# Kernel optimization log

Measured on AMD Instinct MI355X. Metric: run time of the kernel, lower is better.

The kernel has to match this reference:

```python
import jax, jax.numpy as jnp
import numpy as np

NUM_GROUPS = 32
EPS = 1e-6

def group_norm(x, gamma, beta):
    b, c, h, w = x.shape
    xg = x.reshape(b, NUM_GROUPS, c // NUM_GROUPS, h, w)
    mean = xg.mean(axis=(2, 3, 4), keepdims=True)
    var = xg.var(axis=(2, 3, 4), keepdims=True)
    xg = (xg - mean) * jax.lax.rsqrt(var + EPS)
    x = xg.reshape(b, c, h, w)
    return x * gamma[None, :, None, None] + beta[None, :, None, None]

def conv1x1(x, w, b):
    # x: [B,C,H,W], w: [Cout,Cin], b: [Cout]
    return jnp.einsum('bchw,oc->bohw', x, w) + b[None, :, None, None]

def setup_inputs() -> dict:
    key = jax.random.key(0)
    ks = jax.random.split(key, 11)
    B, C, H, W = 4, 512, 64, 64
    s = 1.0 / np.sqrt(C)
    return {
        'x': jax.random.normal(ks[0], (B, C, H, W), dtype=jnp.float32),
        'gn_gamma': jnp.ones((C,), jnp.float32),
        'gn_beta': jnp.zeros((C,), jnp.float32),
        'wq': jax.random.normal(ks[1], (C, C), jnp.float32) * s,
        'bq': jnp.zeros((C,), jnp.float32),
        'wk': jax.random.normal(ks[2], (C, C), jnp.float32) * s,
        'bk': jnp.zeros((C,), jnp.float32),
        'wv': jax.random.normal(ks[3], (C, C), jnp.float32) * s,
        'bv': jnp.zeros((C,), jnp.float32),
        'wo': jax.random.normal(ks[4], (C, C), jnp.float32) * s,
        'bo': jnp.zeros((C,), jnp.float32),
    }

def reference(x, gn_gamma, gn_beta, wq, bq, wk, bk, wv, bv, wo, bo):
    b, c, H, W = x.shape
    h = group_norm(x, gn_gamma, gn_beta)
    q = conv1x1(h, wq, bq).reshape(b, c, H * W).transpose(0, 2, 1)  # [B, HW, C]
    k = conv1x1(h, wk, bk).reshape(b, c, H * W)                      # [B, C, HW]
    v = conv1x1(h, wv, bv).reshape(b, c, H * W).transpose(0, 2, 1)  # [B, HW, C]
    attn = jnp.einsum('bnc,bcm->bnm', q, k) * (c ** -0.5)            # [B, HW, HW]
    attn = jax.nn.softmax(attn, axis=-1)
    out = jnp.einsum('bnm,bmc->bnc', attn, v)                        # [B, HW, C]
    out = out.transpose(0, 2, 1).reshape(b, c, H, W)
    return x + conv1x1(out, wo, bo)
```

## Files before the change

### kernel.cpp

```cpp
#include <hip/hip_runtime.h>
#include <cstdint>
#include <cstddef>

typedef __attribute__((ext_vector_type(8))) short short8;
typedef __attribute__((ext_vector_type(8))) _Float16 half8;
typedef __attribute__((ext_vector_type(4))) float f32x4;
typedef __attribute__((ext_vector_type(16))) float f32x16;

#define C_ 512
#define S_ 4096
#define B_ 4
#define EPS_ 1e-6f
#define SCALE_ 0.04419417382415922f

__device__ __forceinline__ ushort f2bf(float f) {
    union { float f; uint32_t u; } v; v.f = f;
    uint32_t r = v.u + 0x7FFFu + ((v.u >> 16) & 1u);
    return (ushort)(r >> 16);
}

__global__ void wconv_kernel(const float* __restrict__ wq, const float* __restrict__ wk,
                             const float* __restrict__ wv, const float* __restrict__ wo,
                             ushort* __restrict__ out) {
    int i = blockIdx.x * 256 + threadIdx.x;
    out[i]          = f2bf(wq[i]);
    out[262144 + i] = f2bf(wk[i]);
    out[524288 + i] = f2bf(wv[i]);
    out[786432 + i] = f2bf(wo[i]);
}

__global__ __launch_bounds__(512) void gn_stats_kernel(const float* __restrict__ x,
                                                       float* __restrict__ stats) {
    int bg = blockIdx.x;
    const float* xp = x + (size_t)bg * 16 * S_;
    float sum = 0.f, ss = 0.f;
    for (int i = threadIdx.x; i < 16 * S_; i += 512) {
        float v = xp[i];
        sum += v; ss += v * v;
    }
    #pragma unroll
    for (int off = 32; off; off >>= 1) {
        sum += __shfl_down(sum, off);
        ss  += __shfl_down(ss, off);
    }
    __shared__ float r0[8], r1[8];
    int wid = threadIdx.x >> 6;
    if ((threadIdx.x & 63) == 0) { r0[wid] = sum; r1[wid] = ss; }
    __syncthreads();
    if (threadIdx.x == 0) {
        float ts = 0.f, tq = 0.f;
        #pragma unroll
        for (int w = 0; w < 8; w++) { ts += r0[w]; tq += r1[w]; }
        float mean = ts / 65536.f;
        float var  = tq / 65536.f - mean * mean;
        stats[bg * 2]     = mean;
        stats[bg * 2 + 1] = rsqrtf(var + EPS_);
    }
}

__global__ __launch_bounds__(256) void gn_apply_kernel(const float* __restrict__ x,
        const float* __restrict__ gamma, const float* __restrict__ beta,
        const float* __restrict__ stats, ushort* __restrict__ h_t) {
    int sc = blockIdx.x, g = blockIdx.y, b = blockIdx.z;
    int c0 = g * 16;
    int bg = b * 32 + g;
    float mean = stats[bg * 2], rstd = stats[bg * 2 + 1];
    int t = threadIdx.x;
    __shared__ float tile[16][257];
    const float* xp = x + ((size_t)b * C_ + c0) * S_ + sc * 256;
    {
        int c = t >> 4, s0 = (t & 15) * 4;
        const float* src = xp + (size_t)c * S_;
        #pragma unroll
        for (int j = 0; j < 4; j++) {
            float4 d = *(const float4*)(src + s0 + 64 * j);
            tile[c][s0 + 64 * j + 0] = d.x;
            tile[c][s0 + 64 * j + 1] = d.y;
            tile[c][s0 + 64 * j + 2] = d.z;
            tile[c][s0 + 64 * j + 3] = d.w;
        }
    }
    __syncthreads();
    {
        float vv[16];
        #pragma unroll
        for (int ci = 0; ci < 16; ci++) {
            float a = rstd * gamma[c0 + ci];
            float bb2 = beta[c0 + ci] - mean * a;
            vv[ci] = tile[ci][t] * a + bb2;
        }
        uint4 lo, hi;
        lo.x = (uint32_t)f2bf(vv[0])  | ((uint32_t)f2bf(vv[1])  << 16);
        lo.y = (uint32_t)f2bf(vv[2])  | ((uint32_t)f2bf(vv[3])  << 16);
        lo.z = (uint32_t)f2bf(vv[4])  | ((uint32_t)f2bf(vv[5])  << 16);
        lo.w = (uint32_t)f2bf(vv[6])  | ((uint32_t)f2bf(vv[7])  << 16);
        hi.x = (uint32_t)f2bf(vv[8])  | ((uint32_t)f2bf(vv[9])  << 16);
        hi.y = (uint32_t)f2bf(vv[10]) | ((uint32_t)f2bf(vv[11]) << 16);
        hi.z = (uint32_t)f2bf(vv[12]) | ((uint32_t)f2bf(vv[13]) << 16);
        hi.w = (uint32_t)f2bf(vv[14]) | ((uint32_t)f2bf(vv[15]) << 16);
        ushort* dst = h_t + ((size_t)b * S_ + sc * 256 + t) * C_ + c0;
        *(uint4*)dst = lo;
        *(uint4*)(dst + 8) = hi;
    }
}

template <int MODE>
__global__ __launch_bounds__(256, 2) void gemm_kernel(
        const ushort* __restrict__ A,
        const ushort* __restrict__ Bt,
        const float* __restrict__ bias,
        void* __restrict__ outp,
        const float* __restrict__ xres,
        float scale) {
    int bb = blockIdx.z;
    int m0 = blockIdx.y * 128;
    int n0 = blockIdx.x * 128;
    const ushort* Ap = A + (size_t)m0 * 512;
    const ushort* Bp = Bt + (size_t)bb * S_ * C_ + (size_t)n0 * 512;

    extern __shared__ char lds[];

    int t = threadIdx.x, lane = t & 63, wid = t >> 6;
    int l31 = lane & 31, lh = lane >> 5;
    int wm = (wid >> 1) * 64, wn = (wid & 1) * 64;

    f32x16 acc[2][2] = {};

    #define G_STAGE(sbuf, k0)                                                            \
        {                                                                                \
            char* Adst = lds + (sbuf) * 16384;                                           \
            char* Bdst = lds + 32768 + (sbuf) * 16384;                                   \
            _Pragma("unroll")                                                            \
            for (int i_ = 0; i_ < 4; i_++) {                                             \
                int cb = wid * 64 + i_ * 256;                                            \
                int cid = cb + lane;                                                     \
                int row = cid >> 3, c16 = cid & 7;                                       \
                int sw = ((c16 * 16) ^ ((row & 7) << 4));                                \
                const char* sa = (const char*)(Ap + (size_t)row * 512 + (k0)) + sw;      \
                __builtin_amdgcn_global_load_lds(                                        \
                    (const __attribute__((address_space(1))) unsigned int*)sa,           \
                    (__attribute__((address_space(3))) unsigned int*)(Adst + cb * 16),   \
                    16, 0, 0);                                                           \
                const char* sb = (const char*)(Bp + (size_t)row * 512 + (k0)) + sw;      \
                __builtin_amdgcn_global_load_lds(                                        \
                    (const __attribute__((address_space(1))) unsigned int*)sb,           \
                    (__attribute__((address_space(3))) unsigned int*)(Bdst + cb * 16),   \
                    16, 0, 0);                                                           \
            }                                                                            \
        }

    G_STAGE(0, 0);
    asm volatile("s_waitcnt vmcnt(0)" ::: "memory");
    __builtin_amdgcn_s_barrier();
    asm volatile("" ::: "memory");

    for (int k0 = 0; k0 < 512; k0 += 64) {
        int s = (k0 >> 6) & 1;
        if (k0 + 64 < 512) G_STAGE(s ^ 1, k0 + 64);
        char* Al = lds + s * 16384;
        char* Bl = lds + 32768 + s * 16384;
        #pragma unroll
        for (int ks = 0; ks < 4; ks++) {
            short8 af[2], bfr[2];
            #pragma unroll
            for (int i = 0; i < 2; i++) {
                int rowa = wm + i * 32 + l31;
                af[i] = *(const short8*)(Al + rowa * 128 + ((ks * 32 + lh * 16) ^ ((rowa & 7) << 4)));
                int rowb = wn + i * 32 + l31;
                bfr[i] = *(const short8*)(Bl + rowb * 128 + ((ks * 32 + lh * 16) ^ ((rowb & 7) << 4)));
            }
            #pragma unroll
            for (int i = 0; i < 2; i++)
                #pragma unroll
                for (int j = 0; j < 2; j++)
                    acc[i][j] = __builtin_amdgcn_mfma_f32_32x32x16_bf16(af[i], bfr[j], acc[i][j], 0, 0, 0);
        }
        asm volatile("s_waitcnt vmcnt(0) lgkmcnt(0)" ::: "memory");
        __builtin_amdgcn_s_barrier();
        asm volatile("" ::: "memory");
    }
    #undef G_STAGE

    #pragma unroll
    for (int i = 0; i < 2; i++) {
        #pragma unroll
        for (int q = 0; q < 4; q++) {
            int mbase = m0 + wm + i * 32 + q * 8 + 4 * lh;
            float bs[4];
            #pragma unroll
            for (int r = 0; r < 4; r++) bs[r] = bias[mbase + r];
            #pragma unroll
            for (int j = 0; j < 2; j++) {
                int n = n0 + wn + j * 32 + l31;
                if (MODE == 0) {
                    ushort* O = (ushort*)outp + ((size_t)bb * S_ + n) * C_ + mbase;
                    uint2 pp;
                    pp.x = (uint32_t)f2bf((acc[i][j][q * 4 + 0] + bs[0]) * scale) |
                           ((uint32_t)f2bf((acc[i][j][q * 4 + 1] + bs[1]) * scale) << 16);
                    pp.y = (uint32_t)f2bf((acc[i][j][q * 4 + 2] + bs[2]) * scale) |
                           ((uint32_t)f2bf((acc[i][j][q * 4 + 3] + bs[3]) * scale) << 16);
                    *(uint2*)O = pp;
                } else if (MODE == 1) {
                    ushort* O = (ushort*)outp + (size_t)bb * C_ * S_ + (size_t)mbase * S_ + n;
                    #pragma unroll
                    for (int r = 0; r < 4; r++) O[(size_t)r * S_] = f2bf(acc[i][j][q * 4 + r] + bs[r]);
                } else {
                    float* O = (float*)outp + (size_t)bb * C_ * S_ + (size_t)mbase * S_ + n;
                    const float* X = xres + (size_t)bb * C_ * S_ + (size_t)mbase * S_ + n;
                    #pragma unroll
                    for (int r = 0; r < 4; r++)
                        O[(size_t)r * S_] = X[(size_t)r * S_] + acc[i][j][q * 4 + r] + bs[r];
                }
            }
        }
    }
}

#define KBUF_SZ  65536
#define SLDS_OFF 131072
#define PLDS_OFF 149504
#define STM_OFF  158720

__device__ __forceinline__ void stage_k(const ushort* kp, int kv0, int wid, int lane, char* Kbuf) {
    #pragma unroll
    for (int p = 0; p < 8; p++) {
        int row = wid * 8 + p;
        const char* src = (const char*)(kp + (size_t)(kv0 + row) * C_) + ((lane * 16) ^ ((row & 7) << 4));
        __builtin_amdgcn_global_load_lds(
            (const __attribute__((address_space(1))) unsigned int*)src,
            (__attribute__((address_space(3))) unsigned int*)(Kbuf + row * 1024),
            16, 0, 0);
    }
}

__global__ __launch_bounds__(512, 2) void attn_kernel(const ushort* __restrict__ q_t,
        const ushort* __restrict__ k_t, const ushort* __restrict__ v,
        ushort* __restrict__ ao_t) {
    constexpr int NIT = S_ / 64;
    int id = blockIdx.x;
    int bb = (id & 7) >> 1;
    int qb = ((id & 1) << 5) | (id >> 3);
    int s0 = qb * 64;
    const ushort* qp = q_t + (size_t)bb * S_ * C_;
    const ushort* kp = k_t + (size_t)bb * S_ * C_;
    const ushort* vp = v   + (size_t)bb * C_ * S_;

    extern __shared__ char lds[];
    char* Kbuf0 = lds;
    char* Kbuf1 = lds + KBUF_SZ;
    _Float16* S_lds = (_Float16*)(lds + SLDS_OFF);
    char*  P_lds = lds + PLDS_OFF;
    float* st_m  = (float*)(lds + STM_OFF);
    float* st_l  = st_m + 64;
    float* st_f  = st_m + 128;
    int*   rflag = (int*)(st_m + 192);

    int t = threadIdx.x, lane = t & 63, wid = t >> 6;
    int l31 = lane & 31, lh = lane >> 5;
    int qt = (wid >> 2) & 1, nt = (wid >> 1) & 1, ch = wid & 1;

    if (t < 64) { st_m[t] = -1e30f; st_l[t] = 0.f; }
    if (t == 0) *rflag = 0;

    short8 qf[16];
    {
        const ushort* qrow = qp + (size_t)(s0 + qt * 32 + l31) * C_ + ch * 256 + lh * 8;
        #pragma unroll
        for (int ks = 0; ks < 16; ks++)
            qf[ks] = *(const short8*)(qrow + ks * 16);
    }
    f32x16 o_[2][2] = {};

    const ushort* vdb_base = vp + (size_t)(wid * 64 + l31) * S_ + lh * 8;

    stage_k(kp, 0, wid, lane, Kbuf0);
    asm volatile("s_waitcnt vmcnt(0) lgkmcnt(0)" ::: "memory");
    __builtin_amdgcn_s_barrier();
    asm volatile("" ::: "memory");

    for (int it = 0; it < NIT; it++) {
        int kv0 = it * 64;
        char* Kcur = (it & 1) ? Kbuf1 : Kbuf0;
        char* Knxt = (it & 1) ? Kbuf0 : Kbuf1;

        short8 vb[2][4];
        {
            const ushort* vdb = vdb_base + kv0;
            #pragma unroll
            for (int dt = 0; dt < 2; dt++)
                #pragma unroll
                for (int ks2 = 0; ks2 < 4; ks2++)
                    vb[dt][ks2] = *(const short8*)(vdb + (size_t)dt * 32 * S_ + ks2 * 16);
        }
        if (it + 1 < NIT)
            stage_k(kp, kv0 + 64, wid, lane, Knxt);

        f32x16 sacc = {};
        {
            int krow = nt * 32 + l31;
            const char* kb = Kcur + krow * 1024;
            int sw = (krow & 7) << 4;
            int cb0 = ch * 512 + lh * 16;
            #pragma unroll
            for (int ks = 0; ks < 16; ks++) {
                short8 kf = *(const short8*)(kb + ((cb0 + ks * 32) ^ sw));
                sacc = __builtin_amdgcn_mfma_f32_32x32x16_bf16(qf[ks], kf, sacc, 0, 0, 0);
            }
        }
        {
            _Float16* Sp = S_lds + (size_t)ch * 4608 + (size_t)(qt * 32) * 72 + nt * 32 + l31;
            #pragma unroll
            for (int r = 0; r < 16; r++) {
                int qrow = (r & 3) + 8 * (r >> 2) + 4 * lh;
                Sp[qrow * 72] = (_Float16)sacc[r];
            }
        }
        asm volatile("s_waitcnt lgkmcnt(0)" ::: "memory");
        __builtin_amdgcn_s_barrier();
        asm volatile("" ::: "memory");

        {
            int row = t >> 3, j = t & 7;
            half8 h0 = *(const half8*)((const char*)S_lds + (size_t)row * 144 + j * 16);
            half8 h1 = *(const half8*)((const char*)S_lds + 9216 + (size_t)row * 144 + j * 16);
            float sv[8];
            #pragma unroll
            for (int i = 0; i < 8; i++) sv[i] = (float)h0[i] + (float)h1[i];
            float mx = sv[0];
            #pragma unroll
            for (int i = 1; i < 8; i++) mx = fmaxf(mx, sv[i]);
            mx = fmaxf(mx, __shfl_xor(mx, 1));
            mx = fmaxf(mx, __shfl_xor(mx, 2));
            mx = fmaxf(mx, __shfl_xor(mx, 4));
            float mold = st_m[row];
            bool need = (mx > mold + 6.0f);
            float mnew = need ? mx : mold;
            if (need) *rflag = 1;
            float ps = 0.f;
            uint32_t pk[4];
            #pragma unroll
            for (int i = 0; i < 4; i++) {
                float p0 = __expf(sv[2 * i]     - mnew);
                float p1 = __expf(sv[2 * i + 1] - mnew);
                ps += p0 + p1;
                pk[i] = (uint32_t)f2bf(p0) | ((uint32_t)f2bf(p1) << 16);
            }
            *(uint4*)(P_lds + (size_t)row * 144 + j * 16) = *(uint4*)pk;
            ps += __shfl_xor(ps, 1); ps += __shfl_xor(ps, 2); ps += __shfl_xor(ps, 4);
            if (j == 0) {
                float ef = need ? __expf(mold - mnew) : 1.0f;
                if (need) st_m[row] = mnew;
                st_f[row] = ef;
                st_l[row] = st_l[row] * ef + ps;
            }
        }
        asm volatile("s_waitcnt lgkmcnt(0)" ::: "memory");
        __builtin_amdgcn_s_barrier();
        asm volatile("" ::: "memory");

        {
            if (*rflag) {
                #pragma unroll
                for (int qt2 = 0; qt2 < 2; qt2++) {
                    f32x4 f0 = *(const f32x4*)(st_f + qt2 * 32 + 0  + 4 * lh);
                    f32x4 f1 = *(const f32x4*)(st_f + qt2 * 32 + 8  + 4 * lh);
                    f32x4 f2 = *(const f32x4*)(st_f + qt2 * 32 + 16 + 4 * lh);
                    f32x4 f3 = *(const f32x4*)(st_f + qt2 * 32 + 24 + 4 * lh);
                    float fr[16];
                    #pragma unroll
                    for (int e = 0; e < 4; e++) {
                        fr[e] = f0[e]; fr[4 + e] = f1[e]; fr[8 + e] = f2[e]; fr[12 + e] = f3[e];
                    }
                    #pragma unroll
                    for (int dt = 0; dt < 2; dt++)
                        #pragma unroll
                        for (int r = 0; r < 16; r++)
                            o_[qt2][dt][r] *= fr[r];
                }
            }
            short8 pa[2][4];
            #pragma unroll
            for (int qt2 = 0; qt2 < 2; qt2++)
                #pragma unroll
                for (int ks2 = 0; ks2 < 4; ks2++)
                    pa[qt2][ks2] = *(const short8*)(P_lds + (size_t)(qt2 * 32 + l31) * 144 + ks2 * 32 + lh * 16);
            #pragma unroll
            for (int qt2 = 0; qt2 < 2; qt2++)
                #pragma unroll
                for (int dt = 0; dt < 2; dt++)
                    #pragma unroll
                    for (int ks2 = 0; ks2 < 4; ks2++)
                        o_[qt2][dt] = __builtin_amdgcn_mfma_f32_32x32x16_bf16(pa[qt2][ks2], vb[dt][ks2], o_[qt2][dt], 0, 0, 0);
        }
        asm volatile("s_waitcnt vmcnt(0) lgkmcnt(0)" ::: "memory");
        __builtin_amdgcn_s_barrier();
        asm volatile("" ::: "memory");
        if (t == 0) *rflag = 0;
    }

    #pragma unroll
    for (int qt2 = 0; qt2 < 2; qt2++) {
        f32x4 l0 = *(const f32x4*)(st_l + qt2 * 32 + 0  + 4 * lh);
        f32x4 l1 = *(const f32x4*)(st_l + qt2 * 32 + 8  + 4 * lh);
        f32x4 l2 = *(const f32x4*)(st_l + qt2 * 32 + 16 + 4 * lh);
        f32x4 l3 = *(const f32x4*)(st_l + qt2 * 32 + 24 + 4 * lh);
        float rl[16];
        #pragma unroll
        for (int e = 0; e < 4; e++) {
            rl[e] = 1.0f / l0[e]; rl[4 + e] = 1.0f / l1[e];
            rl[8 + e] = 1.0f / l2[e]; rl[12 + e] = 1.0f / l3[e];
        }
        #pragma unroll
        for (int dt = 0; dt < 2; dt++) {
            int d = wid * 64 + dt * 32 + l31;
            #pragma unroll
            for (int r = 0; r < 16; r++) {
                int q = qt2 * 32 + (r & 3) + 8 * (r >> 2) + 4 * lh;
                ao_t[((size_t)bb * S_ + s0 + q) * C_ + d] = f2bf(o_[qt2][dt][r] * rl[r]);
            }
        }
    }
}

extern "C" void kernel_launch(void* const* d_in, const int* in_sizes, int n_in,
                              void* d_out, int out_size, void* d_ws, size_t ws_size,
                              hipStream_t stream) {
    const float* x  = (const float*)d_in[0];
    const float* gg = (const float*)d_in[1];
    const float* gb = (const float*)d_in[2];
    const float* wq = (const float*)d_in[3];
    const float* bq = (const float*)d_in[4];
    const float* wk = (const float*)d_in[5];
    const float* bk = (const float*)d_in[6];
    const float* wv = (const float*)d_in[7];
    const float* bv = (const float*)d_in[8];
    const float* wo = (const float*)d_in[9];
    const float* bo = (const float*)d_in[10];
    float* out = (float*)d_out;

    char* ws = (char*)d_ws;
    const size_t BUF = (size_t)B_ * S_ * C_ * 2;
    ushort* h_t  = (ushort*)(ws);
    ushort* q_t  = (ushort*)(ws + BUF);
    ushort* k_t  = (ushort*)(ws + 2 * BUF);
    ushort* v_n  = (ushort*)(ws + 3 * BUF);
    ushort* ao_t = (ushort*)(ws + 4 * BUF);
    ushort* wb   = (ushort*)(ws + 5 * BUF);
    float* stats = (float*)(ws + 5 * BUF + 4 * 524288);

    wconv_kernel<<<1024, 256, 0, stream>>>(wq, wk, wv, wo, wb);
    gn_stats_kernel<<<128, 512, 0, stream>>>(x, stats);
    gn_apply_kernel<<<dim3(16, 32, B_), 256, 0, stream>>>(x, gg, gb, stats, h_t);

    dim3 ggrid(32, 4, B_);
    gemm_kernel<0><<<ggrid, 256, 65536, stream>>>(wb,          h_t, bq, (void*)q_t, nullptr, SCALE_);
    gemm_kernel<0><<<ggrid, 256, 65536, stream>>>(wb + 262144, h_t, bk, (void*)k_t, nullptr, 1.0f);
    gemm_kernel<1><<<ggrid, 256, 65536, stream>>>(wb + 524288, h_t, bv, (void*)v_n, nullptr, 1.0f);

    attn_kernel<<<256, 512, 159552, stream>>>(q_t, k_t, v_n, ao_t);

    gemm_kernel<2><<<ggrid, 256, 65536, stream>>>(wb + 786432, ao_t, bo, (void*)out, x, 1.0f);
}
```

Baseline: 450.2 us.

## Software-pipeline attention QK with PV across iterations and stage GEMM stores via LDS

The attention loop is restructured so the QK^T score MFMAs for the next KV tile are issued after the PV MFMAs of the current tile, with K prefetched two tiles ahead and a double-buffered rescale flag. This removes one barrier per iteration and is meant to overlap global K loads and score compute with the softmax and PV phases. Separately, the MODE 0 GEMM epilogue (Q and K projections) now writes its tile into swizzled LDS and then emits coalesced 16-byte row stores instead of scattered 8-byte stores. The partial vmcnt waits and the reuse of LDS buffers add correctness risk if the load counts or buffer lifetimes are off.

```diff
diff --git a/kernel.cpp b/kernel.cpp
--- a/kernel.cpp
+++ b/kernel.cpp
@@ -181,26 +181,57 @@
     }
     #undef G_STAGE
 
-    #pragma unroll
-    for (int i = 0; i < 2; i++) {
-        #pragma unroll
-        for (int q = 0; q < 4; q++) {
-            int mbase = m0 + wm + i * 32 + q * 8 + 4 * lh;
-            float bs[4];
-            #pragma unroll
-            for (int r = 0; r < 4; r++) bs[r] = bias[mbase + r];
-            #pragma unroll
-            for (int j = 0; j < 2; j++) {
-                int n = n0 + wn + j * 32 + l31;
-                if (MODE == 0) {
-                    ushort* O = (ushort*)outp + ((size_t)bb * S_ + n) * C_ + mbase;
+    if (MODE == 0) {
+        char* T = lds;
+        #pragma unroll
+        for (int i = 0; i < 2; i++) {
+            #pragma unroll
+            for (int q = 0; q < 4; q++) {
+                int m_l = wm + i * 32 + q * 8 + 4 * lh;
+                float bs[4];
+                #pragma unroll
+                for (int r = 0; r < 4; r++) bs[r] = bias[m0 + m_l + r];
+                #pragma unroll
+                for (int j = 0; j < 2; j++) {
+                    int n_l = wn + j * 32 + l31;
                     uint2 pp;
                     pp.x = (uint32_t)f2bf((acc[i][j][q * 4 + 0] + bs[0]) * scale) |
                            ((uint32_t)f2bf((acc[i][j][q * 4 + 1] + bs[1]) * scale) << 16);
                     pp.y = (uint32_t)f2bf((acc[i][j][q * 4 + 2] + bs[2]) * scale) |
                            ((uint32_t)f2bf((acc[i][j][q * 4 + 3] + bs[3]) * scale) << 16);
-                    *(uint2*)O = pp;
-                } else if (MODE == 1) {
+                    *(uint2*)(T + n_l * 272 + ((m_l * 2) ^ ((n_l & 7) << 4))) = pp;
+                }
+            }
+        }
+        asm volatile("s_waitcnt lgkmcnt(0)" ::: "memory");
+        __builtin_amdgcn_s_barrier();
+        asm volatile("" ::: "memory");
+        {
+            int n_l = t >> 1, mh = (t & 1) * 64;
+            const char* src = T + n_l * 272;
+            int sw = (n_l & 7) << 4;
+            ushort* dst = (ushort*)outp + ((size_t)bb * S_ + n0 + n_l) * C_ + m0 + mh;
+            #pragma unroll
+            for (int k = 0; k < 8; k++) {
+                uint4 d = *(const uint4*)(src + ((mh * 2 + k * 16) ^ sw));
+                *(uint4*)(dst + k * 8) = d;
+            }
+        }
+        return;
+    }
+
+    #pragma unroll
+    for (int i = 0; i < 2; i++) {
+        #pragma unroll
+        for (int q = 0; q < 4; q++) {
+            int mbase = m0 + wm + i * 32 + q * 8 + 4 * lh;
+            float bs[4];
+            #pragma unroll
+            for (int r = 0; r < 4; r++) bs[r] = bias[mbase + r];
+            #pragma unroll
+            for (int j = 0; j < 2; j++) {
+                int n = n0 + wn + j * 32 + l31;
+                if (MODE == 1) {
                     ushort* O = (ushort*)outp + (size_t)bb * C_ * S_ + (size_t)mbase * S_ + n;
                     #pragma unroll
                     for (int r = 0; r < 4; r++) O[(size_t)r * S_] = f2bf(acc[i][j][q * 4 + r] + bs[r]);
@@ -260,7 +291,7 @@
     int qt = (wid >> 2) & 1, nt = (wid >> 1) & 1, ch = wid & 1;
 
     if (t < 64) { st_m[t] = -1e30f; st_l[t] = 0.f; }
-    if (t == 0) *rflag = 0;
+    if (t < 2) rflag[t] = 0;
 
     short8 qf[16];
     {
@@ -270,55 +301,49 @@
             qf[ks] = *(const short8*)(qrow + ks * 16);
     }
     f32x16 o_[2][2] = {};
-
     const ushort* vdb_base = vp + (size_t)(wid * 64 + l31) * S_ + lh * 8;
 
+    #define S_PHASE(KB)                                                                   \
+        {                                                                                 \
+            f32x16 sacc = {};                                                             \
+            int krow = nt * 32 + l31;                                                     \
+            const char* kb = (KB) + krow * 1024;                                          \
+            int sw = (krow & 7) << 4;                                                     \
+            int cb0 = ch * 512 + lh * 16;                                                 \
+            _Pragma("unroll")                                                             \
+            for (int ks = 0; ks < 16; ks++) {                                             \
+                short8 kf = *(const short8*)(kb + ((cb0 + ks * 32) ^ sw));                \
+                sacc = __builtin_amdgcn_mfma_f32_32x32x16_bf16(qf[ks], kf, sacc, 0, 0, 0);\
+            }                                                                             \
+            _Float16* Sp = S_lds + (size_t)ch * 4608 + (size_t)(qt * 32) * 72 + nt * 32 + l31; \
+            _Pragma("unroll")                                                             \
+            for (int r = 0; r < 16; r++) {                                                \
+                int qrow = (r & 3) + 8 * (r >> 2) + 4 * lh;                               \
+                Sp[qrow * 72] = (_Float16)sacc[r];                                        \
+            }                                                                             \
+        }
+
     stage_k(kp, 0, wid, lane, Kbuf0);
-    asm volatile("s_waitcnt vmcnt(0) lgkmcnt(0)" ::: "memory");
+    stage_k(kp, 64, wid, lane, Kbuf1);
+    asm volatile("s_waitcnt vmcnt(8)" ::: "memory");
     __builtin_amdgcn_s_barrier();
     asm volatile("" ::: "memory");
+    S_PHASE(Kbuf0);
+    asm volatile("s_waitcnt lgkmcnt(0)" ::: "memory");
+    __builtin_amdgcn_s_barrier();
+    asm volatile("" ::: "memory");
 
     for (int it = 0; it < NIT; it++) {
-        int kv0 = it * 64;
-        char* Kcur = (it & 1) ? Kbuf1 : Kbuf0;
-        char* Knxt = (it & 1) ? Kbuf0 : Kbuf1;
-
         short8 vb[2][4];
         {
-            const ushort* vdb = vdb_base + kv0;
+            const ushort* vdb = vdb_base + it * 64;
             #pragma unroll
             for (int dt = 0; dt < 2; dt++)
                 #pragma unroll
                 for (int ks2 = 0; ks2 < 4; ks2++)
                     vb[dt][ks2] = *(const short8*)(vdb + (size_t)dt * 32 * S_ + ks2 * 16);
         }
-        if (it + 1 < NIT)
-            stage_k(kp, kv0 + 64, wid, lane, Knxt);
-
-        f32x16 sacc = {};
-        {
-            int krow = nt * 32 + l31;
-            const char* kb = Kcur + krow * 1024;
-            int sw = (krow & 7) << 4;
-            int cb0 = ch * 512 + lh * 16;
-            #pragma unroll
-            for (int ks = 0; ks < 16; ks++) {
-                short8 kf = *(const short8*)(kb + ((cb0 + ks * 32) ^ sw));
-                sacc = __builtin_amdgcn_mfma_f32_32x32x16_bf16(qf[ks], kf, sacc, 0, 0, 0);
-            }
-        }
-        {
-            _Float16* Sp = S_lds + (size_t)ch * 4608 + (size_t)(qt * 32) * 72 + nt * 32 + l31;
-            #pragma unroll
-            for (int r = 0; r < 16; r++) {
-                int qrow = (r & 3) + 8 * (r >> 2) + 4 * lh;
-                Sp[qrow * 72] = (_Float16)sacc[r];
-            }
-        }
-        asm volatile("s_waitcnt lgkmcnt(0)" ::: "memory");
-        __builtin_amdgcn_s_barrier();
-        asm volatile("" ::: "memory");
-
+        if (t == 0 && it > 0) rflag[(it - 1) & 1] = 0;
         {
             int row = t >> 3, j = t & 7;
             half8 h0 = *(const half8*)((const char*)S_lds + (size_t)row * 144 + j * 16);
@@ -335,7 +360,7 @@
             float mold = st_m[row];
             bool need = (mx > mold + 6.0f);
             float mnew = need ? mx : mold;
-            if (need) *rflag = 1;
+            if (need) rflag[it & 1] = 1;
             float ps = 0.f;
             uint32_t pk[4];
             #pragma unroll
@@ -355,29 +380,32 @@
             }
         }
         asm volatile("s_waitcnt lgkmcnt(0)" ::: "memory");
+        asm volatile("s_waitcnt vmcnt(8)" ::: "memory");
         __builtin_amdgcn_s_barrier();
         asm volatile("" ::: "memory");
 
+        if (rflag[it & 1]) {
+            #pragma unroll
+            for (int qt2 = 0; qt2 < 2; qt2++) {
+                f32x4 f0 = *(const f32x4*)(st_f + qt2 * 32 + 0  + 4 * lh);
+                f32x4 f1 = *(const f32x4*)(st_f + qt2 * 32 + 8  + 4 * lh);
+                f32x4 f2 = *(const f32x4*)(st_f + qt2 * 32 + 16 + 4 * lh);
+                f32x4 f3 = *(const f32x4*)(st_f + qt2 * 32 + 24 + 4 * lh);
+                float fr[16];
+                #pragma unroll
+                for (int e = 0; e < 4; e++) {
+                    fr[e] = f0[e]; fr[4 + e] = f1[e]; fr[8 + e] = f2[e]; fr[12 + e] = f3[e];
+                }
+                #pragma unroll
+                for (int dt = 0; dt < 2; dt++)
+                    #pragma unroll
+                    for (int r = 0; r < 16; r++)
+                        o_[qt2][dt][r] *= fr[r];
+            }
+        }
+        if (it + 2 < NIT)
+            stage_k(kp, (it + 2) * 64, wid, lane, (it & 1) ? Kbuf1 : Kbuf0);
         {
-            if (*rflag) {
-                #pragma unroll
-                for (int qt2 = 0; qt2 < 2; qt2++) {
-                    f32x4 f0 = *(const f32x4*)(st_f + qt2 * 32 + 0  + 4 * lh);
-                    f32x4 f1 = *(const f32x4*)(st_f + qt2 * 32 + 8  + 4 * lh);
-                    f32x4 f2 = *(const f32x4*)(st_f + qt2 * 32 + 16 + 4 * lh);
-                    f32x4 f3 = *(const f32x4*)(st_f + qt2 * 32 + 24 + 4 * lh);
-                    float fr[16];
-                    #pragma unroll
-                    for (int e = 0; e < 4; e++) {
-                        fr[e] = f0[e]; fr[4 + e] = f1[e]; fr[8 + e] = f2[e]; fr[12 + e] = f3[e];
-                    }
-                    #pragma unroll
-                    for (int dt = 0; dt < 2; dt++)
-                        #pragma unroll
-                        for (int r = 0; r < 16; r++)
-                            o_[qt2][dt][r] *= fr[r];
-                }
-            }
             short8 pa[2][4];
             #pragma unroll
             for (int qt2 = 0; qt2 < 2; qt2++)
@@ -392,11 +420,13 @@
                     for (int ks2 = 0; ks2 < 4; ks2++)
                         o_[qt2][dt] = __builtin_amdgcn_mfma_f32_32x32x16_bf16(pa[qt2][ks2], vb[dt][ks2], o_[qt2][dt], 0, 0, 0);
         }
-        asm volatile("s_waitcnt vmcnt(0) lgkmcnt(0)" ::: "memory");
+        if (it + 1 < NIT)
+            S_PHASE((it & 1) ? Kbuf0 : Kbuf1);
+        asm volatile("s_waitcnt lgkmcnt(0)" ::: "memory");
         __builtin_amdgcn_s_barrier();
         asm volatile("" ::: "memory");
-        if (t == 0) *rflag = 0;
-    }
+    }
+    #undef S_PHASE
 
     #pragma unroll
     for (int qt2 = 0; qt2 < 2; qt2++) {
@@ -457,7 +487,7 @@
     gemm_kernel<0><<<ggrid, 256, 65536, stream>>>(wb + 262144, h_t, bk, (void*)k_t, nullptr, 1.0f);
     gemm_kernel<1><<<ggrid, 256, 65536, stream>>>(wb + 524288, h_t, bv, (void*)v_n, nullptr, 1.0f);
 
-    attn_kernel<<<256, 512, 159552, stream>>>(q_t, k_t, v_n, ao_t);
+    attn_kernel<<<256, 512, 159560, stream>>>(q_t, k_t, v_n, ao_t);
 
     gemm_kernel<2><<<ggrid, 256, 65536, stream>>>(wb + 786432, ao_t, bo, (void*)out, x, 1.0f);
 }
```

Measured after the change: 484.5 us. 7.6% more time.
